# Kernel optimization log

Hardware: AMD Instinct MI355X
Metric: run time of the kernel (lower is better)

The kernel has to match this reference:

```python
import jax, jax.numpy as jnp
import numpy as np

N, NFEAT, NHID, NCLASS, E = 50000, 256, 64, 40, 800000


def _glorot(key, shape):
    lim = 1.0 / np.sqrt(shape[0])
    return jax.random.uniform(key, shape, jnp.float32, -lim, lim)


def setup_inputs() -> dict:
    key = jax.random.key(0)
    ks = jax.random.split(key, 12)
    x = jax.random.normal(ks[0], (N, NFEAT), jnp.float32)
    edge_src = jax.random.randint(ks[1], (E,), 0, N, jnp.int32)
    edge_dst = jax.random.randint(ks[2], (E,), 0, N, jnp.int32)
    edge_val = jax.random.uniform(ks[3], (E,), jnp.float32)
    eps = jax.random.normal(ks[4], (N, NCLASS), jnp.float32)
    W1 = _glorot(ks[5], (NFEAT, NHID))
    b1 = _glorot(ks[6], (NHID,))
    W11 = _glorot(ks[7], (NHID, NCLASS))
    b11 = _glorot(ks[8], (NCLASS,))
    W12 = _glorot(ks[9], (NHID, NCLASS))
    b12 = _glorot(ks[10], (NCLASS,))
    return {"x": x, "edge_src": edge_src, "edge_dst": edge_dst,
            "edge_val": edge_val, "eps": eps,
            "W1": W1, "b1": b1, "W11": W11, "b11": b11,
            "W12": W12, "b12": b12}


def _spmm(edge_src, edge_dst, edge_val, mat, n):
    # sparse adj (COO) @ dense mat: gather rows at src, weight, scatter-add to dst
    msgs = edge_val[:, None] * mat[edge_src]          # [E, d]
    return jax.ops.segment_sum(msgs, edge_dst, num_segments=n)


def reference(x, edge_src, edge_dst, edge_val, eps, W1, b1, W11, b11, W12, b12):
    n = x.shape[0]
    # gc1: relu(adj @ (x @ W1) + b1)
    h = jax.nn.relu(_spmm(edge_src, edge_dst, edge_val, x @ W1, n) + b1)
    # two parallel heads on the same hidden representation
    mean = _spmm(edge_src, edge_dst, edge_val, h @ W11, n) + b11
    logstd = _spmm(edge_src, edge_dst, edge_val, h @ W12, n) + b12
    # reparameterization trick + log_softmax over classes
    z = eps * jnp.exp(logstd) + mean
    return jax.nn.log_softmax(z, axis=1)
```

## Files before the change

### kernel.cpp

```cpp
#include <hip/hip_runtime.h>
#include <hip/hip_bf16.h>
#include <math.h>

#define NN 50000
#define NFEAT 256
#define NHID 64
#define NCLASS 40
#define EDGES 800000
#define SCAN_BLK 512

#define BM 64
#define BK 32
__global__ __launch_bounds__(256) void k_gemm1(const float* __restrict__ x,
                                               const float* __restrict__ W1,
                                               float* __restrict__ xw) {
    __shared__ float xs[BK][BM + 4];
    __shared__ float ws[BK][NHID];
    const int tid = threadIdx.x;
    const int tx  = tid & 15;
    const int ty  = tid >> 4;
    const int r0  = blockIdx.x * BM;

    float acc[4][4] = {};

    for (int kc = 0; kc < NFEAT; kc += BK) {
        #pragma unroll
        for (int p = 0; p < 2; ++p) {
            int e   = tid * 4 + p * 1024;
            int row = e >> 5;
            int k   = e & 31;
            int gr  = r0 + row;
            float4 v = make_float4(0.f, 0.f, 0.f, 0.f);
            if (gr < NN) v = *(const float4*)&x[(size_t)gr * NFEAT + kc + k];
            xs[k + 0][row] = v.x; xs[k + 1][row] = v.y;
            xs[k + 2][row] = v.z; xs[k + 3][row] = v.w;
        }
        #pragma unroll
        for (int p = 0; p < 2; ++p) {
            int e  = tid * 4 + p * 1024;
            int kk = e >> 6;
            int c  = e & 63;
            *(float4*)&ws[kk][c] = *(const float4*)&W1[(size_t)(kc + kk) * NHID + c];
        }
        __syncthreads();
        #pragma unroll
        for (int kk = 0; kk < BK; ++kk) {
            float4 a = *(const float4*)&xs[kk][ty * 4];
            float4 b = *(const float4*)&ws[kk][tx * 4];
            acc[0][0] += a.x * b.x; acc[0][1] += a.x * b.y; acc[0][2] += a.x * b.z; acc[0][3] += a.x * b.w;
            acc[1][0] += a.y * b.x; acc[1][1] += a.y * b.y; acc[1][2] += a.y * b.z; acc[1][3] += a.y * b.w;
            acc[2][0] += a.z * b.x; acc[2][1] += a.z * b.y; acc[2][2] += a.z * b.z; acc[2][3] += a.z * b.w;
            acc[3][0] += a.w * b.x; acc[3][1] += a.w * b.y; acc[3][2] += a.w * b.z; acc[3][3] += a.w * b.w;
        }
        __syncthreads();
    }
    #pragma unroll
    for (int i = 0; i < 4; ++i) {
        int gr = r0 + ty * 4 + i;
        if (gr < NN)
            *(float4*)&xw[(size_t)gr * NHID + tx * 4] =
                make_float4(acc[i][0], acc[i][1], acc[i][2], acc[i][3]);
    }
}

__global__ void k_zero(int* __restrict__ count) {
    int i = blockIdx.x * 256 + threadIdx.x;
    if (i < NN) count[i] = 0;
}

__global__ void k_hist(const int* __restrict__ dst, int* __restrict__ count) {
    int t = blockIdx.x * 256 + threadIdx.x;
    if (t < EDGES / 4) {
        int4 d = ((const int4*)dst)[t];
        atomicAdd(&count[d.x], 1);
        atomicAdd(&count[d.y], 1);
        atomicAdd(&count[d.z], 1);
        atomicAdd(&count[d.w], 1);
    }
}

__global__ __launch_bounds__(SCAN_BLK) void k_scanA(const int* __restrict__ count,
                                                    int* __restrict__ tmp,
                                                    int* __restrict__ blocksum) {
    __shared__ int s[SCAN_BLK];
    int i = blockIdx.x * SCAN_BLK + threadIdx.x;
    int v = (i < NN) ? count[i] : 0;
    s[threadIdx.x] = v;
    __syncthreads();
    for (int off = 1; off < SCAN_BLK; off <<= 1) {
        int t = (threadIdx.x >= off) ? s[threadIdx.x - off] : 0;
        __syncthreads();
        s[threadIdx.x] += t;
        __syncthreads();
    }
    if (i < NN) tmp[i] = s[threadIdx.x];
    if (threadIdx.x == SCAN_BLK - 1) blocksum[blockIdx.x] = s[SCAN_BLK - 1];
}

__global__ void k_scanB(const int* __restrict__ blocksum, int* __restrict__ blockoff, int nb) {
    __shared__ int s[128];
    int v = (threadIdx.x < nb) ? blocksum[threadIdx.x] : 0;
    s[threadIdx.x] = v;
    __syncthreads();
    for (int off = 1; off < 128; off <<= 1) {
        int t = (threadIdx.x >= off) ? s[threadIdx.x - off] : 0;
        __syncthreads();
        s[threadIdx.x] += t;
        __syncthreads();
    }
    if (threadIdx.x < nb) blockoff[threadIdx.x] = s[threadIdx.x] - v;
}

__global__ void k_scanC(const int* __restrict__ tmp, const int* __restrict__ blockoff,
                        const int* __restrict__ count,
                        int* __restrict__ row_ptr, int* __restrict__ cursor) {
    int i = blockIdx.x * 256 + threadIdx.x;
    if (i < NN) {
        int incl = tmp[i] + blockoff[i / SCAN_BLK];
        row_ptr[i + 1] = incl;
        cursor[i] = incl - count[i];
        if (i == 0) row_ptr[0] = 0;
    }
}

__global__ void k_scatter(const int* __restrict__ src, const int* __restrict__ dst,
                          const float* __restrict__ val, int* __restrict__ cursor,
                          int2* __restrict__ csr) {
    int e = blockIdx.x * 256 + threadIdx.x;
    if (e < EDGES) {
        int p = atomicAdd(&cursor[dst[e]], 1);
        int2 cv;
        cv.x = src[e];
        cv.y = __float_as_int(val[e]);
        csr[p] = cv;
    }
}

template <bool RELU>
__global__ __launch_bounds__(256) void k_spmm(const float* __restrict__ in,
                                              const int* __restrict__ row_ptr,
                                              const int2* __restrict__ csr,
                                              const float* __restrict__ bias,
                                              float* __restrict__ out) {
    const int lane = threadIdx.x & 63;
    int gw = (blockIdx.x * 256 + threadIdx.x) >> 6;
    if (gw >= NN) return;
    const int r   = __builtin_amdgcn_readfirstlane(gw);
    const int beg = row_ptr[r];
    const int end = row_ptr[r + 1];

    float acc0 = 0.f, acc1 = 0.f;
    int j = beg;
    for (; j + 3 < end; j += 4) {
        int2 a = csr[j], b = csr[j + 1], c = csr[j + 2], d = csr[j + 3];
        acc0 += __int_as_float(a.y) * in[(size_t)a.x * NHID + lane];
        acc1 += __int_as_float(b.y) * in[(size_t)b.x * NHID + lane];
        acc0 += __int_as_float(c.y) * in[(size_t)c.x * NHID + lane];
        acc1 += __int_as_float(d.y) * in[(size_t)d.x * NHID + lane];
    }
    for (; j < end; ++j) {
        int2 a = csr[j];
        acc0 += __int_as_float(a.y) * in[(size_t)a.x * NHID + lane];
    }
    float acc = acc0 + acc1;

    if (RELU)
        out[(size_t)r * NHID + lane] = fmaxf(acc + bias[lane], 0.f);
    else
        out[(size_t)r * NHID + lane] = acc;
}

__global__ __launch_bounds__(256) void k_final(const float* __restrict__ g2,
                                               const float* __restrict__ W11,
                                               const float* __restrict__ b11,
                                               const float* __restrict__ W12,
                                               const float* __restrict__ b12,
                                               const float* __restrict__ eps,
                                               float* __restrict__ out) {
    __shared__ float W11l[NHID * NCLASS];
    __shared__ float W12l[NHID * NCLASS];
    __shared__ float bl[2 * NCLASS];
    for (int i = threadIdx.x; i < NHID * NCLASS; i += 256) {
        W11l[i] = W11[i];
        W12l[i] = W12[i];
    }
    if (threadIdx.x < NCLASS) bl[threadIdx.x] = b11[threadIdx.x];
    else if (threadIdx.x < 2 * NCLASS) bl[threadIdx.x] = b12[threadIdx.x - NCLASS];
    __syncthreads();

    const int lane = threadIdx.x & 63;
    const int gw   = (blockIdx.x * 256 + threadIdx.x) >> 6;
    const bool act = lane < NCLASS;
    const int  cc  = act ? lane : NCLASS - 1;

    const int r0 = gw * 4;
    if (r0 >= NN) return;
    const int ur = __builtin_amdgcn_readfirstlane(r0);
    const float* __restrict__ g = g2 + (size_t)ur * NHID;

    float m[4], lg[4];
    #pragma unroll
    for (int i = 0; i < 4; ++i) { m[i] = bl[cc]; lg[i] = bl[NCLASS + cc]; }

    #pragma unroll 4
    for (int k = 0; k < NHID; ++k) {
        float w1 = W11l[k * NCLASS + cc];
        float w2 = W12l[k * NCLASS + cc];
        float ga = g[k], gb = g[NHID + k], gc = g[2 * NHID + k], gd = g[3 * NHID + k];
        m[0] += ga * w1; lg[0] += ga * w2;
        m[1] += gb * w1; lg[1] += gb * w2;
        m[2] += gc * w1; lg[2] += gc * w2;
        m[3] += gd * w1; lg[3] += gd * w2;
    }

    float z[4];
    #pragma unroll
    for (int i = 0; i < 4; ++i)
        z[i] = act ? (eps[(size_t)(ur + i) * NCLASS + lane] * expf(lg[i]) + m[i]) : -1e30f;

    float zmax[4], s[4];
    #pragma unroll
    for (int i = 0; i < 4; ++i) zmax[i] = z[i];
    #pragma unroll
    for (int off = 32; off >= 1; off >>= 1) {
        #pragma unroll
        for (int i = 0; i < 4; ++i) zmax[i] = fmaxf(zmax[i], __shfl_xor(zmax[i], off));
    }
    #pragma unroll
    for (int i = 0; i < 4; ++i) s[i] = act ? expf(z[i] - zmax[i]) : 0.f;
    #pragma unroll
    for (int off = 32; off >= 1; off >>= 1) {
        #pragma unroll
        for (int i = 0; i < 4; ++i) s[i] += __shfl_xor(s[i], off);
    }
    if (act) {
        #pragma unroll
        for (int i = 0; i < 4; ++i)
            out[(size_t)(ur + i) * NCLASS + lane] = z[i] - zmax[i] - logf(s[i]);
    }
}

extern "C" void kernel_launch(void* const* d_in, const int* in_sizes, int n_in,
                              void* d_out, int out_size, void* d_ws, size_t ws_size,
                              hipStream_t stream) {
    const float* x        = (const float*)d_in[0];
    const int*   edge_src = (const int*)d_in[1];
    const int*   edge_dst = (const int*)d_in[2];
    const float* edge_val = (const float*)d_in[3];
    const float* eps      = (const float*)d_in[4];
    const float* W1       = (const float*)d_in[5];
    const float* b1       = (const float*)d_in[6];
    const float* W11      = (const float*)d_in[7];
    const float* b11      = (const float*)d_in[8];
    const float* W12      = (const float*)d_in[9];
    const float* b12      = (const float*)d_in[10];
    float* out = (float*)d_out;

    int2*  csr     = (int2*)d_ws;
    float* xw      = (float*)(csr + EDGES);
    float* h       = xw + (size_t)NN * NHID;
    int*   count   = (int*)(h + (size_t)NN * NHID);
    int*   tmp     = count + NN;
    int*   row_ptr = tmp + NN;
    int*   cursor  = row_ptr + (NN + 1);
    int*   blocksum= cursor + NN;
    int*   blockoff= blocksum + 128;
    float* g2 = xw;

    const int NB = (NN + SCAN_BLK - 1) / SCAN_BLK;

    k_gemm1<<<(NN + BM - 1) / BM, 256, 0, stream>>>(x, W1, xw);
    k_zero<<<(NN + 255) / 256, 256, 0, stream>>>(count);
    k_hist<<<(EDGES / 4 + 255) / 256, 256, 0, stream>>>(edge_dst, count);
    k_scanA<<<NB, SCAN_BLK, 0, stream>>>(count, tmp, blocksum);
    k_scanB<<<1, 128, 0, stream>>>(blocksum, blockoff, NB);
    k_scanC<<<(NN + 255) / 256, 256, 0, stream>>>(tmp, blockoff, count, row_ptr, cursor);
    k_scatter<<<(EDGES + 255) / 256, 256, 0, stream>>>(edge_src, edge_dst, edge_val,
                                                       cursor, csr);
    k_spmm<true><<<NN / 4, 256, 0, stream>>>(xw, row_ptr, csr, b1, h);
    k_spmm<false><<<NN / 4, 256, 0, stream>>>(h, row_ptr, csr, nullptr, g2);
    k_final<<<(NN / 4 + 3) / 4, 256, 0, stream>>>(g2, W11, b11, W12, b12, eps, out);
}
```

Baseline: 309.7 us.

## Replace atomic CSR scatter with two-pass bucketed scatter via staging buffer

Swaps the per-edge global-atomic CSR scatter for two passes. The first pass buckets edges into groups of 32 destination nodes, with blocks split by residue class so each block touches a subset of buckets. The second pass places each bucket's edges into final CSR slots using shared-memory atomics. The aim is to cut global atomic contention and random scatter traffic. The cost is an extra kernel, an extra read and write of the staging buffer (which reuses the h region), and every chunk being read 8 times.

```diff
diff --git a/kernel.cpp b/kernel.cpp
--- a/kernel.cpp
+++ b/kernel.cpp
@@ -8,6 +8,11 @@
 #define NCLASS 40
 #define EDGES 800000
 #define SCAN_BLK 512
+
+#define W_BKT 32
+#define K_BKT ((NN + W_BKT - 1) / W_BKT)
+#define CHUNK 1600
+#define NCHUNK ((EDGES + CHUNK - 1) / CHUNK)
 
 #define BM 64
 #define BK 32
@@ -113,26 +118,54 @@
 
 __global__ void k_scanC(const int* __restrict__ tmp, const int* __restrict__ blockoff,
                         const int* __restrict__ count,
-                        int* __restrict__ row_ptr, int* __restrict__ cursor) {
+                        int* __restrict__ row_ptr, int* __restrict__ bcur) {
     int i = blockIdx.x * 256 + threadIdx.x;
     if (i < NN) {
         int incl = tmp[i] + blockoff[i / SCAN_BLK];
         row_ptr[i + 1] = incl;
-        cursor[i] = incl - count[i];
         if (i == 0) row_ptr[0] = 0;
-    }
-}
-
-__global__ void k_scatter(const int* __restrict__ src, const int* __restrict__ dst,
-                          const float* __restrict__ val, int* __restrict__ cursor,
-                          int2* __restrict__ csr) {
-    int e = blockIdx.x * 256 + threadIdx.x;
-    if (e < EDGES) {
-        int p = atomicAdd(&cursor[dst[e]], 1);
-        int2 cv;
-        cv.x = src[e];
-        cv.y = __float_as_int(val[e]);
-        csr[p] = cv;
+        if ((i & (W_BKT - 1)) == 0) bcur[i / W_BKT] = incl - count[i];
+    }
+}
+
+__global__ __launch_bounds__(256) void k_scat1(const int* __restrict__ src,
+                                               const int* __restrict__ dst,
+                                               const float* __restrict__ val,
+                                               int* __restrict__ bcur,
+                                               int2* __restrict__ staging) {
+    const int res   = blockIdx.x & 7;
+    const int base  = (blockIdx.x >> 3) * CHUNK;
+    const int end   = min(base + CHUNK, EDGES);
+    for (int e = base + threadIdx.x; e < end; e += 256) {
+        int d = dst[e];
+        int b = d >> 5;
+        if ((b & 7) == res) {
+            int p = atomicAdd(&bcur[b], 1);
+            int2 cv;
+            cv.x = src[e] | ((d & (W_BKT - 1)) << 17);
+            cv.y = __float_as_int(val[e]);
+            staging[p] = cv;
+        }
+    }
+}
+
+__global__ __launch_bounds__(256) void k_scat2(const int* __restrict__ row_ptr,
+                                               const int2* __restrict__ staging,
+                                               int2* __restrict__ csr) {
+    __shared__ int cur[W_BKT];
+    const int nb = blockIdx.x * W_BKT;
+    if (threadIdx.x < W_BKT) {
+        int node = nb + threadIdx.x;
+        cur[threadIdx.x] = (node < NN) ? row_ptr[node] : 0;
+    }
+    __syncthreads();
+    const int beg = row_ptr[nb];
+    const int end = row_ptr[min(nb + W_BKT, NN)];
+    for (int i = beg + threadIdx.x; i < end; i += 256) {
+        int2 cv = staging[i];
+        int dl = cv.x >> 17;
+        int p  = atomicAdd(&cur[dl], 1);
+        csr[p] = make_int2(cv.x & 0x1FFFF, cv.y);
     }
 }
 
@@ -259,11 +292,12 @@
     int2*  csr     = (int2*)d_ws;
     float* xw      = (float*)(csr + EDGES);
     float* h       = xw + (size_t)NN * NHID;
+    int2*  staging = (int2*)h;
     int*   count   = (int*)(h + (size_t)NN * NHID);
     int*   tmp     = count + NN;
     int*   row_ptr = tmp + NN;
-    int*   cursor  = row_ptr + (NN + 1);
-    int*   blocksum= cursor + NN;
+    int*   bcur    = row_ptr + (NN + 1);
+    int*   blocksum= bcur + K_BKT;
     int*   blockoff= blocksum + 128;
     float* g2 = xw;
 
@@ -274,9 +308,9 @@
     k_hist<<<(EDGES / 4 + 255) / 256, 256, 0, stream>>>(edge_dst, count);
     k_scanA<<<NB, SCAN_BLK, 0, stream>>>(count, tmp, blocksum);
     k_scanB<<<1, 128, 0, stream>>>(blocksum, blockoff, NB);
-    k_scanC<<<(NN + 255) / 256, 256, 0, stream>>>(tmp, blockoff, count, row_ptr, cursor);
-    k_scatter<<<(EDGES + 255) / 256, 256, 0, stream>>>(edge_src, edge_dst, edge_val,
-                                                       cursor, csr);
+    k_scanC<<<(NN + 255) / 256, 256, 0, stream>>>(tmp, blockoff, count, row_ptr, bcur);
+    k_scat1<<<NCHUNK * 8, 256, 0, stream>>>(edge_src, edge_dst, edge_val, bcur, staging);
+    k_scat2<<<K_BKT, 256, 0, stream>>>(row_ptr, staging, csr);
     k_spmm<true><<<NN / 4, 256, 0, stream>>>(xw, row_ptr, csr, b1, h);
     k_spmm<false><<<NN / 4, 256, 0, stream>>>(h, row_ptr, csr, nullptr, g2);
     k_final<<<(NN / 4 + 3) / 4, 256, 0, stream>>>(g2, W11, b11, W12, b12, eps, out);
```

Result: slower. 426.0 us (+37.5%).
